# Performance work log

Measured on AMD Instinct MI355X. Metric: run time of the kernel, lower is better.

The kernel has to match this reference:

```python
import jax, jax.numpy as jnp
import numpy as np

B, T, V, D, DH, H = 4, 512, 32000, 768, 768, 4  # batch, seq, vocab, dim_in, dim_out(per-head & ffn), heads


def layer_norm(x, g, b, eps=1e-5):
    m = jnp.mean(x, axis=-1, keepdims=True)
    v = jnp.mean((x - m) ** 2, axis=-1, keepdims=True)
    return (x - m) * jax.lax.rsqrt(v + eps) * g + b


def setup_inputs() -> dict:
    key = jax.random.key(0)
    ks = jax.random.split(key, 20)
    s = 0.02
    f = lambda k, shp: (jax.random.normal(k, shp, jnp.float32) * s)
    return {
        "x": jax.random.randint(ks[0], (B, T), 0, V),
        "attention_mask": jax.random.randint(ks[1], (B, 1, T), 0, 2).astype(bool),
        "token_embed": f(ks[2], (V, D)),
        "segment_embed": f(ks[3], (V, D)),
        "ln_embed_g": jnp.ones((D,), jnp.float32), "ln_embed_b": jnp.zeros((D,), jnp.float32),
        "Wq": f(ks[4], (H, D, DH)), "bq": f(ks[5], (H, DH)),
        "Wk": f(ks[6], (H, D, DH)), "bk": f(ks[7], (H, DH)),
        "Wv": f(ks[8], (H, D, DH)), "bv": f(ks[9], (H, DH)),
        "Wo": f(ks[10], (H * DH, D)), "bo": f(ks[11], (D,)),
        "ln_attn_g": jnp.ones((D,), jnp.float32), "ln_attn_b": jnp.zeros((D,), jnp.float32),
        "W1": f(ks[12], (D, DH)), "b1": f(ks[13], (DH,)),
        "W2": f(ks[14], (DH, D)), "b2": f(ks[15], (D,)),
        "ln_enc_g": jnp.ones((D,), jnp.float32), "ln_enc_b": jnp.zeros((D,), jnp.float32),
        "Wproj": f(ks[16], (D, V)), "bproj": f(ks[17], (V,)),
        "Wcls": f(ks[18], (D, 2)), "bcls": f(ks[19], (2,)),
    }


def reference(x, attention_mask, token_embed, segment_embed, ln_embed_g, ln_embed_b,
              Wq, bq, Wk, bk, Wv, bv, Wo, bo, ln_attn_g, ln_attn_b,
              W1, b1, W2, b2, ln_enc_g, ln_enc_b, Wproj, bproj, Wcls, bcls):
    Bsz, Tlen = x.shape
    dim = token_embed.shape[1]
    # JointEmbedding: segment tensor is 0 for first half, 1 afterwards
    seg = jnp.zeros_like(x).at[:, Tlen // 2 + 1:].set(1)
    # positional encoding (faithful to source: exponent is 2*j/dim per column j,
    # sin on even columns, cos on odd columns, applied to pos/10000**exp)
    d = 2.0 * jnp.arange(dim, dtype=jnp.float32) / dim            # [D]
    p = jnp.arange(Tlen, dtype=jnp.float32)[:, None] / (10000.0 ** d)  # [T, D]
    pe = jnp.where(jnp.arange(dim) % 2 == 0, jnp.sin(p), jnp.cos(p))   # [T, D]
    emb = token_embed[x] + segment_embed[seg] + pe[None]          # [B, T, D]
    emb = layer_norm(emb, ln_embed_g, ln_embed_b)

    # Multi-head attention (vectorized over the per-head Python loop)
    Q = jnp.einsum('btd,hde->bhte', emb, Wq) + bq[None, :, None, :]
    K = jnp.einsum('btd,hde->bhte', emb, Wk) + bk[None, :, None, :]
    Vh = jnp.einsum('btd,hde->bhte', emb, Wv) + bv[None, :, None, :]
    # NOTE: source scales by seq_len**-0.5 (Q.size(1)), not head_dim**-0.5
    scores = jnp.einsum('bhte,bhse->bhts', Q, K) * (float(Tlen) ** -0.5)
    # NOTE: source masked_fill_'s with value 1e-9 (not -inf) before softmax
    scores = jnp.where(attention_mask[:, None, :, :], 1e-9, scores)
    attn = jax.nn.softmax(scores, axis=-1)
    ctx = jnp.einsum('bhts,bhse->bhte', attn, Vh)                 # [B, H, T, DH]
    cat = ctx.transpose(0, 2, 1, 3).reshape(Bsz, Tlen, -1)        # head concat order
    attn_out = layer_norm(cat @ Wo + bo, ln_attn_g, ln_attn_b)

    # FFN (no residual in source; dropout is identity at inference)
    h = jax.nn.gelu(attn_out @ W1 + b1, approximate=False)
    enc = layer_norm(h @ W2 + b2, ln_enc_g, ln_enc_b)

    token_pred = enc @ Wproj + bproj                              # [B, T, V]
    logits = jax.nn.log_softmax(token_pred, axis=-1)
    cls_out = enc[:, 0, :] @ Wcls + bcls                          # [B, 2]
    return logits, cls_out
```

## Files before the change

### kernel.cpp

```cpp
#include <hip/hip_runtime.h>
#include <hip/hip_bf16.h>
#include <stdint.h>

#define B_ 4
#define T_ 512
#define V_ 32000
#define D_ 768
#define DH_ 768
#define H_ 4
#define R_ 2048

typedef unsigned short u16;
typedef __attribute__((ext_vector_type(4))) float f32x4;
typedef __attribute__((ext_vector_type(8))) short s16x8;
typedef __attribute__((ext_vector_type(8))) unsigned short u16x8;
typedef __attribute__((address_space(3))) char* lds_cp;
typedef const __attribute__((address_space(1))) char* gl_cp;

__device__ __forceinline__ float bf2f(u16 u){
  union { float f; unsigned int i; } w; w.i = ((unsigned int)u) << 16; return w.f;
}
__device__ __forceinline__ u16 f2bf(float f){
  union { float f; unsigned int i; } w; w.f = f;
  unsigned int r = w.i + 0x7fffu + ((w.i >> 16) & 1u);
  return (u16)(r >> 16);
}

__device__ __forceinline__ float block_sum(float v, float* red){
  #pragma unroll
  for (int o = 32; o; o >>= 1) v += __shfl_down(v, o);
  __syncthreads();
  if ((threadIdx.x & 63) == 0) red[threadIdx.x >> 6] = v;
  __syncthreads();
  return red[0] + red[1] + red[2] + red[3];
}
__device__ __forceinline__ float block_max(float v, float* red){
  #pragma unroll
  for (int o = 32; o; o >>= 1) v = fmaxf(v, __shfl_down(v, o));
  __syncthreads();
  if ((threadIdx.x & 63) == 0) red[threadIdx.x >> 6] = v;
  __syncthreads();
  return fmaxf(fmaxf(red[0], red[1]), fmaxf(red[2], red[3]));
}

__global__ void mask_convert(const void* __restrict__ mraw, int* __restrict__ mout){
  __shared__ int isbyte;
  if (threadIdx.x == 0) isbyte = 0;
  __syncthreads();
  const unsigned char* by = (const unsigned char*)mraw;
  int f = 0;
  for (int i = threadIdx.x; i < 2048; i += 256)
    if ((i & 3) && by[i]) f = 1;
  if (f) atomicOr(&isbyte, 1);
  __syncthreads();
  if (isbyte){
    for (int i = threadIdx.x; i < 2048; i += 256) mout[i] = by[i] ? 1 : 0;
  } else {
    const int* mi = (const int*)mraw;
    for (int i = threadIdx.x; i < 2048; i += 256) mout[i] = mi[i] ? 1 : 0;
  }
}

__global__ __launch_bounds__(256)
void transpose_all(const float* __restrict__ Wq, const float* __restrict__ Wk,
                   const float* __restrict__ Wv, const float* __restrict__ Wo,
                   const float* __restrict__ W1, const float* __restrict__ W2,
                   u16* __restrict__ wqT, u16* __restrict__ wkT,
                   u16* __restrict__ wvT, u16* __restrict__ woT,
                   u16* __restrict__ w1T, u16* __restrict__ w2T){
  __shared__ u16 tile[32][33];
  int z = blockIdx.z;
  const float* in; u16* out; int out_ld = 768;
  if (z < 4)      { in = Wq + (long)z * 589824;        out = wqT + (long)z * 589824; }
  else if (z < 8) { int k = z - 4;  in = Wk + (long)k * 589824; out = wkT + (long)k * 589824; }
  else if (z < 12){ int k = z - 8;  in = Wv + (long)k * 589824; out = wvT + (long)k * 589824; }
  else if (z < 16){ int k = z - 12; in = Wo + (long)k * 589824; out = woT + (long)k * 768; out_ld = 3072; }
  else if (z == 16){ in = W1; out = w1T; }
  else             { in = W2; out = w2T; }
  int c0 = blockIdx.x * 32, r0 = blockIdx.y * 32;
  int tx = threadIdx.x & 31, ty = threadIdx.x >> 5;
  #pragma unroll
  for (int i = 0; i < 32; i += 8)
    tile[ty + i][tx] = f2bf(in[(long)(r0 + ty + i) * 768 + (c0 + tx)]);
  __syncthreads();
  #pragma unroll
  for (int i = 0; i < 32; i += 8)
    out[(long)(c0 + ty + i) * out_ld + (r0 + tx)] = tile[tx][ty + i];
}

__global__ __launch_bounds__(256)
void transpose_f2b(const float* __restrict__ in, u16* __restrict__ out, int R, int C){
  __shared__ u16 tile[32][33];
  int c0 = blockIdx.x * 32, r0 = blockIdx.y * 32;
  int tx = threadIdx.x & 31, ty = threadIdx.x >> 5;
  #pragma unroll
  for (int i = 0; i < 32; i += 8)
    tile[ty + i][tx] = f2bf(in[(long)(r0 + ty + i) * C + (c0 + tx)]);
  __syncthreads();
  #pragma unroll
  for (int i = 0; i < 32; i += 8)
    out[(long)(c0 + ty + i) * R + (r0 + tx)] = tile[tx][ty + i];
}

__global__ __launch_bounds__(256)
void embed_ln(const int* __restrict__ x, const float* __restrict__ tok,
              const float* __restrict__ seg, const float* __restrict__ g,
              const float* __restrict__ bb, u16* __restrict__ emb){
  __shared__ float red[4];
  int r = blockIdx.x, t = r & 511;
  int tid = threadIdx.x;
  long trow = (long)x[r] * D_;
  long srow = (t > 256) ? (long)D_ : 0;
  float v[3];
  float s = 0.f;
  #pragma unroll
  for (int q = 0; q < 3; ++q){
    int j = tid + q * 256;
    float d = (2.0f * (float)j) * (1.0f / 768.0f);
    float p = (float)t * powf(10000.0f, -d);
    float pe = (j & 1) ? cosf(p) : sinf(p);
    v[q] = tok[trow + j] + seg[srow + j] + pe;
    s += v[q];
  }
  float mean = block_sum(s, red) * (1.0f / 768.0f);
  float vs = 0.f;
  #pragma unroll
  for (int q = 0; q < 3; ++q){ float dd = v[q] - mean; vs += dd * dd; }
  float var = block_sum(vs, red) * (1.0f / 768.0f);
  float inv = rsqrtf(var + 1e-5f);
  #pragma unroll
  for (int q = 0; q < 3; ++q){
    int j = tid + q * 256;
    emb[(long)r * D_ + j] = f2bf((v[q] - mean) * inv * g[j] + bb[j]);
  }
}

__global__ __launch_bounds__(256)
void ln_rows(const u16* __restrict__ in, const float* __restrict__ g,
             const float* __restrict__ bb, u16* __restrict__ out){
  __shared__ float red[4];
  long r = blockIdx.x;
  int tid = threadIdx.x;
  const u16* row = in + r * D_;
  float v[3];
  float s = 0.f;
  #pragma unroll
  for (int q = 0; q < 3; ++q){ v[q] = bf2f(row[tid + q * 256]); s += v[q]; }
  float mean = block_sum(s, red) * (1.0f / 768.0f);
  float vs = 0.f;
  #pragma unroll
  for (int q = 0; q < 3; ++q){ float dd = v[q] - mean; vs += dd * dd; }
  float var = block_sum(vs, red) * (1.0f / 768.0f);
  float inv = rsqrtf(var + 1e-5f);
  #pragma unroll
  for (int q = 0; q < 3; ++q){
    int j = tid + q * 256;
    out[r * D_ + j] = f2bf((v[q] - mean) * inv * g[j] + bb[j]);
  }
}

__global__ __launch_bounds__(256)
void attn_softmax(u16* __restrict__ S, const int* __restrict__ mask){
  __shared__ float red[4];
  int t = blockIdx.x, z = blockIdx.y, b = z >> 2;
  u16* row = S + (long)z * (T_ * T_) + (long)t * T_;
  int tid = threadIdx.x;
  int s0 = tid, s1 = tid + 256;
  float v0 = mask[b * T_ + s0] ? 1e-9f : bf2f(row[s0]);
  float v1 = mask[b * T_ + s1] ? 1e-9f : bf2f(row[s1]);
  float mx = block_max(fmaxf(v0, v1), red);
  float e0 = expf(v0 - mx), e1 = expf(v1 - mx);
  float l = block_sum(e0 + e1, red);
  float inv = 1.0f / l;
  row[s0] = f2bf(e0 * inv);
  row[s1] = f2bf(e1 * inv);
}

__global__ __launch_bounds__(256)
void lsm_b2f(const u16* __restrict__ pred, float* __restrict__ out){
  __shared__ float sm[256], sl[256];
  long r = blockIdx.x;
  const u16x8* rv = (const u16x8*)(pred + r * (long)V_);
  int tid = threadIdx.x;
  float m = -1e30f, l = 0.f;
  for (int c = tid; c < V_ / 8; c += 256){
    u16x8 v = rv[c];
    #pragma unroll
    for (int j = 0; j < 8; ++j){
      float x = bf2f(v[j]);
      if (x > m){ l = l * expf(m - x) + 1.0f; m = x; }
      else l += expf(x - m);
    }
  }
  sm[tid] = m; sl[tid] = l;
  __syncthreads();
  #pragma unroll
  for (int s = 128; s; s >>= 1){
    if (tid < s){
      float m2 = sm[tid + s], l2 = sl[tid + s];
      float M = fmaxf(sm[tid], m2);
      sl[tid] = sl[tid] * expf(sm[tid] - M) + l2 * expf(m2 - M);
      sm[tid] = M;
    }
    __syncthreads();
  }
  float lse = sm[0] + logf(sl[0]);
  f32x4* orow = (f32x4*)(out + r * (long)V_);
  for (int c = tid; c < V_ / 8; c += 256){
    u16x8 v = rv[c];
    f32x4 o0, o1;
    #pragma unroll
    for (int j = 0; j < 4; ++j){ o0[j] = bf2f(v[j]) - lse; o1[j] = bf2f(v[j + 4]) - lse; }
    orow[2 * c] = o0; orow[2 * c + 1] = o1;
  }
}

__global__ __launch_bounds__(256)
void log_softmax_rows(float* __restrict__ tp){
  __shared__ float sm[256], sl[256];
  long r = blockIdx.x;
  float* row = tp + r * (long)V_;
  f32x4* rv = (f32x4*)row;
  int tid = threadIdx.x;
  float m = -1e30f, l = 0.f;
  for (int c = tid; c < V_ / 4; c += 256){
    f32x4 v = rv[c];
    #pragma unroll
    for (int j = 0; j < 4; ++j){
      float x = v[j];
      if (x > m){ l = l * expf(m - x) + 1.0f; m = x; }
      else l += expf(x - m);
    }
  }
  sm[tid] = m; sl[tid] = l;
  __syncthreads();
  #pragma unroll
  for (int s = 128; s; s >>= 1){
    if (tid < s){
      float m2 = sm[tid + s], l2 = sl[tid + s];
      float M = fmaxf(sm[tid], m2);
      sl[tid] = sl[tid] * expf(sm[tid] - M) + l2 * expf(m2 - M);
      sm[tid] = M;
    }
    __syncthreads();
  }
  float lse = sm[0] + logf(sl[0]);
  for (int c = tid; c < V_ / 4; c += 256){
    f32x4 v = rv[c];
    #pragma unroll
    for (int j = 0; j < 4; ++j) v[j] -= lse;
    rv[c] = v;
  }
}

__global__ __launch_bounds__(256)
void cls_head(const u16* __restrict__ enc, const float* __restrict__ Wc,
              const float* __restrict__ bc, float* __restrict__ out){
  int w = threadIdx.x >> 6, lane = threadIdx.x & 63;
  const u16* e = enc + (long)w * (T_ * D_);
  float a0 = 0.f, a1 = 0.f;
  for (int k = lane; k < D_; k += 64){
    float ev = bf2f(e[k]);
    a0 += ev * Wc[k * 2 + 0];
    a1 += ev * Wc[k * 2 + 1];
  }
  #pragma unroll
  for (int o = 32; o; o >>= 1){ a0 += __shfl_down(a0, o); a1 += __shfl_down(a1, o); }
  if (lane == 0){
    out[(long)B_ * T_ * V_ + w * 2 + 0] = a0 + bc[0];
    out[(long)B_ * T_ * V_ + w * 2 + 1] = a1 + bc[1];
  }
}

template<int GELU, int F32OUT>
__global__ __launch_bounds__(256, 2)
void gemm_bt(const u16* __restrict__ A, const u16* __restrict__ Bt,
             const float* __restrict__ bias, void* __restrict__ Cv,
             int lda, int ldb,
             long sAzb, long sAzh, long sBzb, long sBzh, long sbz,
             long sCzb, long sCzh, long sCb, long sCr, long sCc,
             int zsh, float scale, int nt){
  extern __shared__ char smem[];
  u16* sA = (u16*)smem;
  u16* sB = sA + 2 * 128 * 64;
  int tid = threadIdx.x, lane = tid & 63, wid = tid >> 6;
  int wm = wid >> 1, wn = wid & 1;
  int lrow = lane & 15, lquad = lane >> 4;

  unsigned gx = gridDim.x, gy = gridDim.y;
  unsigned nwg = gx * gy * gridDim.z;
  unsigned id = blockIdx.x + gx * (blockIdx.y + gy * blockIdx.z);
  unsigned qq = nwg >> 3, rr = nwg & 7, xcd = id & 7, loc = id >> 3;
  unsigned nid = (xcd < rr ? xcd * (qq + 1) : rr * (qq + 1) + (xcd - rr) * qq) + loc;
  unsigned bx = nid % gx, tmpq = nid / gx;
  unsigned by = tmpq % gy, bz = tmpq / gy;

  int z = (int)bz, zb = z >> zsh, zh = z & ((1 << zsh) - 1);
  long bm = (long)bx * 128, bn = (long)by * 128;
  const u16* Az = A + zb * sAzb + zh * sAzh;
  const u16* Bz = Bt + zb * sBzb + zh * sBzh;

  f32x4 acc[4][4] = {};

  auto stage = [&](int buf, int kt){
    #pragma unroll
    for (int q = 0; q < 4; ++q){
      int seg = wid * 4 + q;
      int idx = seg * 64 + lane;
      int r = idx >> 3, c = idx & 7;
      int ksw = (c ^ (r & 7)) << 3;
      const u16* srcA = Az + (bm + r) * lda + kt * 64 + ksw;
      const u16* srcB = Bz + (bn + r) * ldb + kt * 64 + ksw;
      __builtin_amdgcn_global_load_lds((gl_cp)srcA,
          (lds_cp)((char*)(sA + buf * 8192) + seg * 1024), 16, 0, 0);
      __builtin_amdgcn_global_load_lds((gl_cp)srcB,
          (lds_cp)((char*)(sB + buf * 8192) + seg * 1024), 16, 0, 0);
    }
  };

  stage(0, 0);
  __syncthreads();
  int cur = 0;
  for (int t = 0; t < nt; ++t){
    if (t + 1 < nt) stage(cur ^ 1, t + 1);
    const u16* a0 = sA + cur * 8192;
    const u16* b0 = sB + cur * 8192;
    #pragma unroll
    for (int kk = 0; kk < 2; ++kk){
      int koff = (((kk * 4 + lquad) ^ (lrow & 7)) << 3);
      s16x8 af[4], bfv[4];
      #pragma unroll
      for (int m = 0; m < 4; ++m)
        af[m] = *(const s16x8*)(a0 + (wm * 64 + m * 16 + lrow) * 64 + koff);
      #pragma unroll
      for (int n = 0; n < 4; ++n)
        bfv[n] = *(const s16x8*)(b0 + (wn * 64 + n * 16 + lrow) * 64 + koff);
      #pragma unroll
      for (int m = 0; m < 4; ++m)
        #pragma unroll
        for (int n = 0; n < 4; ++n)
          acc[m][n] = __builtin_amdgcn_mfma_f32_16x16x32_bf16(af[m], bfv[n], acc[m][n], 0, 0, 0);
    }
    __syncthreads();
    cur ^= 1;
  }

  long czbase = zb * sCzb + zh * sCzh;
  #pragma unroll
  for (int n = 0; n < 4; ++n){
    long col = bn + wn * 64 + n * 16 + lrow;
    float bv = bias ? bias[zb * sbz + col] : 0.f;
    #pragma unroll
    for (int m = 0; m < 4; ++m){
      #pragma unroll
      for (int j = 0; j < 4; ++j){
        long row = bm + wm * 64 + m * 16 + lquad * 4 + j;
        float v = acc[m][n][j] * scale + bv;
        if (GELU) v = 0.5f * v * (1.0f + erff(v * 0.70710678118654752f));
        long ci = czbase + (row >> 9) * sCb + (row & 511) * sCr + col * sCc;
        if (F32OUT) ((float*)Cv)[ci] = v;
        else        ((u16*)Cv)[ci] = f2bf(v);
      }
    }
  }
}

template<int F32OUT>
__global__ __launch_bounds__(256, 4)
void gemm_wp(const u16* __restrict__ A, const u16* __restrict__ Bt,
             const float* __restrict__ bias, void* __restrict__ Cv){
  __shared__ char smem[32768];
  const int tid = threadIdx.x, lane = tid & 63, wid = tid >> 6;
  const int wm = wid >> 1, wn = wid & 1;
  const int lrow = lane & 15, lquad = lane >> 4;

  unsigned id = blockIdx.x + 16u * blockIdx.y;
  unsigned wg = (id & 7u) * 500u + (id >> 3);
  const long bm = (long)(wg & 15u) * 128;
  const long bn = (long)(wg >> 4) * 128;
  const int NT = 24;

  f32x4 acc[4][4] = {};

  auto stage = [&](int slot, int kt){
    #pragma unroll
    for (int q = 0; q < 2; ++q){
      int idx = q * 256 + tid;
      int r = idx >> 2, c = idx & 3;
      int lc = c ^ ((r >> 1) & 3);
      const u16* srcA = A + (bm + r) * 768 + kt * 32 + lc * 8;
      const u16* srcB = Bt + (bn + r) * 768 + kt * 32 + lc * 8;
      __builtin_amdgcn_global_load_lds((gl_cp)srcA,
          (lds_cp)(smem + slot * 16384 + idx * 16), 16, 0, 0);
      __builtin_amdgcn_global_load_lds((gl_cp)srcB,
          (lds_cp)(smem + slot * 16384 + 8192 + idx * 16), 16, 0, 0);
    }
  };

  stage(0, 0);
  __syncthreads();
  const int koff = (lquad ^ ((lrow >> 1) & 3)) * 16;
  int cur = 0;
  for (int t = 0; t < NT; ++t){
    if (t + 1 < NT) stage(cur ^ 1, t + 1);
    const char* a0 = smem + cur * 16384;
    const char* b0 = a0 + 8192;
    s16x8 af[4], bfv[4];
    #pragma unroll
    for (int m = 0; m < 4; ++m)
      af[m] = *(const s16x8*)(a0 + (wm * 64 + m * 16 + lrow) * 64 + koff);
    #pragma unroll
    for (int n = 0; n < 4; ++n)
      bfv[n] = *(const s16x8*)(b0 + (wn * 64 + n * 16 + lrow) * 64 + koff);
    #pragma unroll
    for (int m = 0; m < 4; ++m)
      #pragma unroll
      for (int n = 0; n < 4; ++n)
        acc[m][n] = __builtin_amdgcn_mfma_f32_16x16x32_bf16(af[m], bfv[n], acc[m][n], 0, 0, 0);
    __syncthreads();
    cur ^= 1;
  }

  #pragma unroll
  for (int n = 0; n < 4; ++n){
    long col = bn + wn * 64 + n * 16 + lrow;
    float bv = bias[col];
    #pragma unroll
    for (int m = 0; m < 4; ++m){
      #pragma unroll
      for (int j = 0; j < 4; ++j){
        long row = bm + wm * 64 + m * 16 + lquad * 4 + j;
        float v = acc[m][n][j] + bv;
        if (F32OUT) ((float*)Cv)[row * (long)V_ + col] = v;
        else        ((u16*)Cv)[row * (long)V_ + col] = f2bf(v);
      }
    }
  }
}

extern "C" void kernel_launch(void* const* d_in, const int* in_sizes, int n_in,
                              void* d_out, int out_size, void* d_ws, size_t ws_size,
                              hipStream_t stream){
  const int*   x     = (const int*)d_in[0];
  const void*  amask = d_in[1];
  const float* tok = (const float*)d_in[2];
  const float* seg = (const float*)d_in[3];
  const float* lng = (const float*)d_in[4];
  const float* lnb = (const float*)d_in[5];
  const float* Wq  = (const float*)d_in[6];
  const float* bq  = (const float*)d_in[7];
  const float* Wk  = (const float*)d_in[8];
  const float* bk  = (const float*)d_in[9];
  const float* Wv  = (const float*)d_in[10];
  const float* bv  = (const float*)d_in[11];
  const float* Wo  = (const float*)d_in[12];
  const float* bo  = (const float*)d_in[13];
  const float* lag = (const float*)d_in[14];
  const float* lab = (const float*)d_in[15];
  const float* W1  = (const float*)d_in[16];
  const float* b1  = (const float*)d_in[17];
  const float* W2  = (const float*)d_in[18];
  const float* b2  = (const float*)d_in[19];
  const float* leg = (const float*)d_in[20];
  const float* leb = (const float*)d_in[21];
  const float* Wp  = (const float*)d_in[22];
  const float* bp  = (const float*)d_in[23];
  const float* Wc  = (const float*)d_in[24];
  const float* bc  = (const float*)d_in[25];
  float* out = (float*)d_out;
  char* ws = (char*)d_ws;

  size_t off = 0;
  auto alloc = [&](size_t bytes){ size_t o = off; off += (bytes + 255) & ~(size_t)255; return o; };
  size_t o_mask = alloc(2048 * 4);
  size_t o_emb  = alloc((size_t)R_ * D_ * 2);
  size_t o_wqT  = alloc((size_t)H_ * D_ * DH_ * 2);
  size_t o_wkT  = alloc((size_t)H_ * D_ * DH_ * 2);
  size_t o_wvT  = alloc((size_t)H_ * D_ * DH_ * 2);
  size_t o_woT  = alloc((size_t)3072 * 768 * 2);
  size_t o_w1T  = alloc((size_t)768 * 768 * 2);
  size_t o_w2T  = alloc((size_t)768 * 768 * 2);
  size_t o_Q    = alloc((size_t)B_ * H_ * T_ * DH_ * 2);
  size_t o_K    = alloc((size_t)B_ * H_ * T_ * DH_ * 2);
  size_t o_VT   = alloc((size_t)B_ * H_ * DH_ * T_ * 2);
  size_t o_S    = alloc((size_t)B_ * H_ * T_ * T_ * 2);
  size_t o_cat  = alloc((size_t)R_ * 3072 * 2);
  size_t o_ap   = alloc((size_t)R_ * D_ * 2);
  size_t o_ao   = alloc((size_t)R_ * D_ * 2);
  size_t o_h1   = alloc((size_t)R_ * D_ * 2);
  size_t o_ep   = alloc((size_t)R_ * D_ * 2);
  size_t o_enc  = alloc((size_t)R_ * D_ * 2);
  size_t o_wpT  = o_Q;
  size_t off_base = off;
  size_t o_pred = alloc((size_t)R_ * V_ * 2);
  int bigws = (ws_size >= off);
  if (ws_size < off_base) return;

  int* maskI = (int*)(ws + o_mask);
  u16* emb  = (u16*)(ws + o_emb);
  u16* wqT  = (u16*)(ws + o_wqT);
  u16* wkT  = (u16*)(ws + o_wkT);
  u16* wvT  = (u16*)(ws + o_wvT);
  u16* woT  = (u16*)(ws + o_woT);
  u16* w1T  = (u16*)(ws + o_w1T);
  u16* w2T  = (u16*)(ws + o_w2T);
  u16* Qb   = (u16*)(ws + o_Q);
  u16* Kb   = (u16*)(ws + o_K);
  u16* VTb  = (u16*)(ws + o_VT);
  u16* Sb   = (u16*)(ws + o_S);
  u16* catb = (u16*)(ws + o_cat);
  u16* apb  = (u16*)(ws + o_ap);
  u16* aob  = (u16*)(ws + o_ao);
  u16* h1b  = (u16*)(ws + o_h1);
  u16* epb  = (u16*)(ws + o_ep);
  u16* encb = (u16*)(ws + o_enc);
  u16* wpT  = (u16*)(ws + o_wpT);
  u16* predb = (u16*)(ws + o_pred);

  const long sQK_zb = (long)H_ * T_ * DH_;
  const long sQK_zh = (long)T_ * DH_;

  mask_convert<<<1, 256, 0, stream>>>(amask, maskI);
  transpose_all<<<dim3(24, 24, 18), 256, 0, stream>>>(Wq, Wk, Wv, Wo, W1, W2,
      wqT, wkT, wvT, woT, w1T, w2T);
  embed_ln<<<R_, 256, 0, stream>>>(x, tok, seg, lng, lnb, emb);

  gemm_bt<0,0><<<dim3(16, 6, 4), 256, 65536, stream>>>(emb, wqT, bq, Qb,
      768, 768, 0, 0, (long)768 * 768, 0, 768,
      sQK_zh, 0, sQK_zb, 768, 1, 0, 1.0f, 12);
  gemm_bt<0,0><<<dim3(16, 6, 4), 256, 65536, stream>>>(emb, wkT, bk, Kb,
      768, 768, 0, 0, (long)768 * 768, 0, 768,
      sQK_zh, 0, sQK_zb, 768, 1, 0, 1.0f, 12);
  gemm_bt<0,0><<<dim3(16, 6, 4), 256, 65536, stream>>>(emb, wvT, bv, VTb,
      768, 768, 0, 0, (long)768 * 768, 0, 768,
      sQK_zh, 0, sQK_zb, 1, 512, 0, 1.0f, 12);

  gemm_bt<0,0><<<dim3(4, 4, 16), 256, 65536, stream>>>(Qb, Kb, nullptr, Sb,
      768, 768, sQK_zb, sQK_zh, sQK_zb, sQK_zh, 0,
      (long)H_ * T_ * T_, (long)T_ * T_, 0, 512, 1, 2, 0.044194173824159216f, 12);

  attn_softmax<<<dim3(512, 16), 256, 0, stream>>>(Sb, maskI);

  gemm_bt<0,0><<<dim3(4, 6, 16), 256, 65536, stream>>>(Sb, VTb, nullptr, catb,
      512, 512, (long)H_ * T_ * T_, (long)T_ * T_, sQK_zb, sQK_zh, 0,
      (long)T_ * 3072, 768, 0, 3072, 1, 2, 1.0f, 8);

  gemm_bt<0,0><<<dim3(16, 6, 1), 256, 65536, stream>>>(catb, woT, bo, apb,
      3072, 3072, 0, 0, 0, 0, 0,
      0, 0, (long)512 * 768, 768, 1, 0, 1.0f, 48);
  ln_rows<<<R_, 256, 0, stream>>>(apb, lag, lab, aob);

  gemm_bt<1,0><<<dim3(16, 6, 1), 256, 65536, stream>>>(aob, w1T, b1, h1b,
      768, 768, 0, 0, 0, 0, 0,
      0, 0, (long)512 * 768, 768, 1, 0, 1.0f, 12);
  gemm_bt<0,0><<<dim3(16, 6, 1), 256, 65536, stream>>>(h1b, w2T, b2, epb,
      768, 768, 0, 0, 0, 0, 0,
      0, 0, (long)512 * 768, 768, 1, 0, 1.0f, 12);
  ln_rows<<<R_, 256, 0, stream>>>(epb, leg, leb, encb);

  transpose_f2b<<<dim3(1000, 24, 1), 256, 0, stream>>>(Wp, wpT, 768, 32000);

  if (bigws){
    gemm_wp<0><<<dim3(16, 250), 256, 0, stream>>>(encb, wpT, bp, predb);
    lsm_b2f<<<R_, 256, 0, stream>>>(predb, out);
  } else {
    gemm_wp<1><<<dim3(16, 250), 256, 0, stream>>>(encb, wpT, bp, out);
    log_softmax_rows<<<R_, 256, 0, stream>>>(out);
  }
  cls_head<<<1, 256, 0, stream>>>(encb, Wc, bc, out);

  (void)in_sizes; (void)n_in; (void)out_size;
}
```

Measured before the change: 502.8 us.

## Load vocab-projection B fragments directly to registers and hand-pipeline A via LDS

Result: slower. 576.4 us (+14.6%).

```diff
diff --git a/kernel.cpp b/kernel.cpp
--- a/kernel.cpp
+++ b/kernel.cpp
@@ -369,7 +369,7 @@
 __global__ __launch_bounds__(256, 4)
 void gemm_wp(const u16* __restrict__ A, const u16* __restrict__ Bt,
              const float* __restrict__ bias, void* __restrict__ Cv){
-  __shared__ char smem[32768];
+  __shared__ char smem[16384];
   const int tid = threadIdx.x, lane = tid & 63, wid = tid >> 6;
   const int wm = wid >> 1, wn = wid & 1;
   const int lrow = lane & 15, lquad = lane >> 4;
@@ -382,43 +382,69 @@
 
   f32x4 acc[4][4] = {};
 
-  auto stage = [&](int slot, int kt){
+  auto stageA = [&](int slot, int kt){
     #pragma unroll
     for (int q = 0; q < 2; ++q){
       int idx = q * 256 + tid;
       int r = idx >> 2, c = idx & 3;
       int lc = c ^ ((r >> 1) & 3);
-      const u16* srcA = A + (bm + r) * 768 + kt * 32 + lc * 8;
-      const u16* srcB = Bt + (bn + r) * 768 + kt * 32 + lc * 8;
-      __builtin_amdgcn_global_load_lds((gl_cp)srcA,
-          (lds_cp)(smem + slot * 16384 + idx * 16), 16, 0, 0);
-      __builtin_amdgcn_global_load_lds((gl_cp)srcB,
-          (lds_cp)(smem + slot * 16384 + 8192 + idx * 16), 16, 0, 0);
+      const u16* src = A + (bm + r) * 768 + kt * 32 + lc * 8;
+      __builtin_amdgcn_global_load_lds((gl_cp)src,
+          (lds_cp)(smem + slot * 8192 + idx * 16), 16, 0, 0);
     }
   };
 
-  stage(0, 0);
-  __syncthreads();
+  unsigned voff[4];
+  #pragma unroll
+  for (int nf = 0; nf < 4; ++nf)
+    voff[nf] = (unsigned)((bn + wn * 64 + nf * 16 + lrow) * 768 * 2);
+
+  s16x8 b0[4], b1[4];
+  auto loadB = [&](s16x8* bq, int kt){
+    unsigned co = (unsigned)(kt * 64 + lquad * 16);
+    #pragma unroll
+    for (int nf = 0; nf < 4; ++nf){
+      asm volatile("global_load_dwordx4 %0, %1, %2"
+                   : "=v"(bq[nf])
+                   : "v"(voff[nf] + co), "s"(Bt));
+    }
+  };
+
   const int koff = (lquad ^ ((lrow >> 1) & 3)) * 16;
-  int cur = 0;
-  for (int t = 0; t < NT; ++t){
-    if (t + 1 < NT) stage(cur ^ 1, t + 1);
-    const char* a0 = smem + cur * 16384;
-    const char* b0 = a0 + 8192;
-    s16x8 af[4], bfv[4];
+  auto tileCompute = [&](int slot, const s16x8* bq){
+    const char* a0 = smem + slot * 8192;
+    s16x8 af[4];
     #pragma unroll
     for (int m = 0; m < 4; ++m)
       af[m] = *(const s16x8*)(a0 + (wm * 64 + m * 16 + lrow) * 64 + koff);
-    #pragma unroll
-    for (int n = 0; n < 4; ++n)
-      bfv[n] = *(const s16x8*)(b0 + (wn * 64 + n * 16 + lrow) * 64 + koff);
+    asm volatile("s_waitcnt lgkmcnt(0)" ::: "memory");
+    __builtin_amdgcn_sched_barrier(0);
+    __builtin_amdgcn_s_setprio(1);
     #pragma unroll
     for (int m = 0; m < 4; ++m)
       #pragma unroll
       for (int n = 0; n < 4; ++n)
-        acc[m][n] = __builtin_amdgcn_mfma_f32_16x16x32_bf16(af[m], bfv[n], acc[m][n], 0, 0, 0);
-    __syncthreads();
-    cur ^= 1;
+        acc[m][n] = __builtin_amdgcn_mfma_f32_16x16x32_bf16(af[m], bq[n], acc[m][n], 0, 0, 0);
+    __builtin_amdgcn_s_setprio(0);
+    __builtin_amdgcn_sched_barrier(0);
+    __builtin_amdgcn_s_barrier();
+  };
+
+  stageA(0, 0); loadB(b0, 0);
+  stageA(1, 1); loadB(b1, 1);
+
+  for (int t = 0; t < NT; t += 2){
+    asm volatile("s_waitcnt vmcnt(6)" ::: "memory");
+    __builtin_amdgcn_sched_barrier(0);
+    __builtin_amdgcn_s_barrier();
+    tileCompute(0, b0);
+    if (t + 2 < NT){ stageA(0, t + 2); loadB(b0, t + 2); }
+    if (t + 2 < NT){ asm volatile("s_waitcnt vmcnt(6)" ::: "memory"); }
+    else           { asm volatile("s_waitcnt vmcnt(0)" ::: "memory"); }
+    __builtin_amdgcn_sched_barrier(0);
+    __builtin_amdgcn_s_barrier();
+    tileCompute(1, b1);
+    if (t + 3 < NT){ stageA(1, t + 3); loadB(b1, t + 3); }
   }
 
   #pragma unroll
```
